# Kernel tuning notes

Measured on AMD Instinct MI355X. Metric: run time of the kernel, lower is better.

The kernel has to match this reference:

```python
import jax, jax.numpy as jnp
import numpy as np

D = 1024      # model_dim
H = 16        # n_heads
BLOCK = 256   # block_dim
B, S = 4, 4096


def setup_inputs() -> dict:
    key = jax.random.key(0)
    ks = jax.random.split(key, 6)
    x = jax.random.normal(ks[0], (B, S, D), dtype=jnp.float32)
    # random permutation per batch row (mirrors torch.argsort(torch.rand(...)))
    rand_perm = jnp.argsort(jax.random.uniform(ks[1], (B, S)), axis=-1).astype(jnp.int32)
    W_in = jax.random.normal(ks[2], (D, 3 * D), dtype=jnp.float32) / np.float32(np.sqrt(D))
    b_in = jax.random.normal(ks[3], (3 * D,), dtype=jnp.float32) * 0.02
    W_out = jax.random.normal(ks[4], (D, D), dtype=jnp.float32) / np.float32(np.sqrt(D))
    b_out = jax.random.normal(ks[5], (D,), dtype=jnp.float32) * 0.02
    return {"x": x, "rand_perm": rand_perm, "W_in": W_in, "b_in": b_in,
            "W_out": W_out, "b_out": b_out}


def reference(x, rand_perm, W_in, b_in, W_out, b_out):
    Bb, Ss, Dm = x.shape
    dh = Dm // H
    nb = Ss // BLOCK  # S divisible by BLOCK -> no padding needed
    # permute sequence: x_rand[..., i, :] = x[..., perm[i], :]
    x_r = jnp.take_along_axis(x, rand_perm[..., None], axis=-2)          # [B,S,D]
    xb = x_r.reshape(Bb, nb, BLOCK, Dm)                                   # block-diagonal chunks
    qkv = jnp.einsum('bntd,de->bnte', xb, W_in) + b_in                    # [B,nb,blk,3D]
    # torch layout: chunk by head first, then (q,k,v) within head
    qkv = qkv.reshape(Bb, nb, BLOCK, H, 3, dh)
    q = jnp.moveaxis(qkv[..., 0, :], 3, 2)                                # [B,nb,H,blk,dh]
    k = jnp.moveaxis(qkv[..., 1, :], 3, 2)
    v = jnp.moveaxis(qkv[..., 2, :], 3, 2)
    scores = jnp.einsum('bnhtd,bnhsd->bnhts', q, k) / np.float32(np.sqrt(dh))
    att = jax.nn.softmax(scores, axis=-1)
    o = jnp.einsum('bnhts,bnhsd->bnhtd', att, v)                          # [B,nb,H,blk,dh]

    def merge(t):  # [B,nb,H,blk,dh] -> [B,S,D] (heads concatenated on feature dim)
        return jnp.moveaxis(t, 2, 3).reshape(Bb, Ss, Dm)

    o = merge(o) @ W_out + b_out
    k_f = merge(k)
    v_f = merge(v)
    # scatter back: out[perm[i]] = src[i]  <=>  out[j] = src[inv_perm[j]]
    inv = jnp.argsort(rand_perm, axis=-1)
    unperm = lambda t: jnp.take_along_axis(t, inv[..., None], axis=-2)
    return unperm(o), unperm(k_f), unperm(v_f)
```

## Files before the change

kernel.cpp:

```cpp
#include <hip/hip_runtime.h>

#define D_   1024
#define H_   16
#define DHd  64
#define BLK  256
#define B_   4
#define S_   4096
#define NB_  16
#define M_   16384
#define N1_  3072
#define NT_  32

typedef __attribute__((ext_vector_type(8))) short short8;
typedef __attribute__((ext_vector_type(4))) float f32x4;
typedef unsigned short u16;
typedef __attribute__((ext_vector_type(4))) unsigned short u16x4;

__device__ inline u16 f2bf(float f) {
  unsigned int u = __float_as_uint(f);
  unsigned int r = (u + 0x7fffu + ((u >> 16) & 1u)) >> 16;
  return (u16)r;
}

__device__ inline void async_ld16(const void* g, void* l) {
  __builtin_amdgcn_global_load_lds(
      (const __attribute__((address_space(1))) unsigned int*)g,
      (__attribute__((address_space(3))) unsigned int*)l, 16, 0, 0);
}

__global__ __launch_bounds__(256)
void permute_cast_kernel(const float* __restrict__ x, const int* __restrict__ perm,
                         u16* __restrict__ xp) {
  int bid = blockIdx.x;
  int b = bid >> 12;
  int i = bid & 4095;
  int prow = perm[b * S_ + i];
  const float4* src = reinterpret_cast<const float4*>(x + (size_t)(b * S_ + prow) * D_);
  float4 v = src[threadIdx.x];
  u16x4 o;
  o.x = f2bf(v.x); o.y = f2bf(v.y); o.z = f2bf(v.z); o.w = f2bf(v.w);
  reinterpret_cast<u16x4*>(xp + (size_t)bid * D_)[threadIdx.x] = o;
}

__global__ __launch_bounds__(256)
void transpose_cast_kernel(const float* __restrict__ src, u16* __restrict__ dst,
                           int R, int C) {
  __shared__ float tile[32][33];
  int tx = threadIdx.x, ty = threadIdx.y;
  int c0 = blockIdx.x * 32, r0 = blockIdx.y * 32;
  #pragma unroll
  for (int i = ty; i < 32; i += 8)
    tile[i][tx] = src[(size_t)(r0 + i) * C + c0 + tx];
  __syncthreads();
  #pragma unroll
  for (int i = ty; i < 32; i += 8)
    dst[(size_t)(c0 + i) * R + r0 + tx] = f2bf(tile[tx][i]);
}

template<int MODE>
__global__ __launch_bounds__(512, 2)
void gemm_kernel(const u16* __restrict__ A, const u16* __restrict__ BT,
                 const float* __restrict__ bias, const int* __restrict__ perm,
                 u16* __restrict__ q_ws, u16* __restrict__ k_ws, u16* __restrict__ vT_ws,
                 float* __restrict__ out_k, float* __restrict__ out_v,
                 float* __restrict__ out_o) {
  constexpr int NCOL = (MODE == 0) ? N1_ : D_;
  constexpr int NWG  = (M_ / 256) * (NCOL / 256);
  constexpr int CPX  = NWG / 8;

  __shared__ u16 LDS[4 * 16384];
  __shared__ int perm_l[256];

  const int tid  = threadIdx.x;
  const int lane = tid & 63;
  const int w    = tid >> 6;
  const int wr   = w >> 2, wc = w & 3;
  const int l4   = lane >> 4, l15 = lane & 15;

  const int orig = blockIdx.x;
  const int lid  = (orig & 7) * CPX + (orig >> 3);
  const int i0   = (lid & 63) * 256;
  const int n0   = (lid >> 6) * 256;
  const int bidx = i0 >> 12;

  if (tid < 256) perm_l[tid] = perm[bidx * S_ + (i0 & 4095) + tid];

  const int srow = tid >> 2;
  const int sq   = (tid & 3) ^ ((tid >> 3) & 3);
  const u16* pA0 = A  + (size_t)(i0 + srow) * 1024 + sq * 8;
  const u16* pA1 = pA0 + (size_t)128 * 1024;
  const u16* pB0 = BT + (size_t)(n0 + srow) * 1024 + sq * 8;
  const u16* pB1 = pB0 + (size_t)128 * 1024;

  const int ps   = l4 ^ ((l15 >> 1) & 3);
  const int aoff = (wr * 128 + l15) * 64 + ps * 16;
  const int boff = 16384 + (wc * 64 + l15) * 64 + ps * 16;

  f32x4 acc[8][4] = {};

  #define STAGE(kt, b) do {                                    \
    const int ko_ = (kt) * 32;                                 \
    u16* base_ = &LDS[(b) * 16384 + w * 512];                  \
    async_ld16(pA0 + ko_, base_);                              \
    async_ld16(pA1 + ko_, base_ + 4096);                       \
    async_ld16(pB0 + ko_, base_ + 8192);                       \
    async_ld16(pB1 + ko_, base_ + 12288);                      \
  } while (0)

  #define COMPUTE(b) do {                                                         \
    const char* lb_ = (const char*)LDS + (b) * 32768;                             \
    short8 af_[8], bf_[4];                                                        \
    _Pragma("unroll")                                                             \
    for (int m = 0; m < 8; ++m)                                                   \
      af_[m] = *reinterpret_cast<const short8*>(lb_ + aoff + m * 1024);           \
    bf_[0] = *reinterpret_cast<const short8*>(lb_ + boff);                        \
    bf_[1] = *reinterpret_cast<const short8*>(lb_ + boff + 1024);                 \
    __builtin_amdgcn_s_setprio(1);                                                \
    _Pragma("unroll")                                                             \
    for (int m = 0; m < 8; ++m) {                                                 \
      acc[m][0] = __builtin_amdgcn_mfma_f32_16x16x32_bf16(af_[m], bf_[0], acc[m][0], 0, 0, 0); \
      acc[m][1] = __builtin_amdgcn_mfma_f32_16x16x32_bf16(af_[m], bf_[1], acc[m][1], 0, 0, 0); \
    }                                                                             \
    __builtin_amdgcn_s_setprio(0);                                                \
    bf_[2] = *reinterpret_cast<const short8*>(lb_ + boff + 2048);                 \
    bf_[3] = *reinterpret_cast<const short8*>(lb_ + boff + 3072);                 \
    __builtin_amdgcn_s_setprio(1);                                                \
    _Pragma("unroll")                                                             \
    for (int m = 0; m < 8; ++m) {                                                 \
      acc[m][2] = __builtin_amdgcn_mfma_f32_16x16x32_bf16(af_[m], bf_[2], acc[m][2], 0, 0, 0); \
      acc[m][3] = __builtin_amdgcn_mfma_f32_16x16x32_bf16(af_[m], bf_[3], acc[m][3], 0, 0, 0); \
    }                                                                             \
    __builtin_amdgcn_s_setprio(0);                                                \
  } while (0)

  STAGE(0, 0);
  STAGE(1, 1);
  #pragma unroll 1
  for (int kt = 0; kt < NT_ - 2; ++kt) {
    STAGE(kt + 2, (kt + 2) & 3);
    asm volatile("s_waitcnt vmcnt(8) lgkmcnt(0)" ::: "memory");
    __builtin_amdgcn_s_barrier();
    COMPUTE(kt & 3);
  }
  asm volatile("s_waitcnt vmcnt(4) lgkmcnt(0)" ::: "memory");
  __builtin_amdgcn_s_barrier();
  COMPUTE((NT_ - 2) & 3);
  asm volatile("s_waitcnt vmcnt(0) lgkmcnt(0)" ::: "memory");
  __builtin_amdgcn_s_barrier();
  COMPUTE((NT_ - 1) & 3);
  #undef STAGE
  #undef COMPUTE

  if (MODE == 0) {
    #pragma unroll
    for (int n = 0; n < 4; ++n) {
      int col = n0 + wc * 64 + n * 16 + l15;
      float bias_v = bias[col];
      int h  = col / 192;
      int rem = col - h * 192;
      int cc = rem >> 6;
      int dd = rem & 63;
      int qcol = (h << 6) + dd;
      #pragma unroll
      for (int m = 0; m < 8; ++m) {
        int rbase = i0 + wr * 128 + m * 16 + l4 * 4;
        if (cc == 0) {
          #pragma unroll
          for (int r = 0; r < 4; ++r) {
            float val = acc[m][n][r] + bias_v;
            q_ws[(size_t)(rbase + r) * D_ + qcol] = f2bf(val);
          }
        } else if (cc == 1) {
          #pragma unroll
          for (int r = 0; r < 4; ++r) {
            float val = acc[m][n][r] + bias_v;
            int rr = rbase + r;
            k_ws[(size_t)rr * D_ + qcol] = f2bf(val);
            int prow = perm_l[rr - i0];
            out_k[(size_t)(bidx * S_ + prow) * D_ + qcol] = val;
          }
        } else {
          u16x4 pk;
          #pragma unroll
          for (int r = 0; r < 4; ++r) {
            float val = acc[m][n][r] + bias_v;
            int rr = rbase + r;
            int prow = perm_l[rr - i0];
            out_v[(size_t)(bidx * S_ + prow) * D_ + qcol] = val;
            pk[r] = f2bf(val);
          }
          int i_loc = rbase & 4095;
          int nblk = i_loc >> 8;
          int t    = i_loc & 255;
          *reinterpret_cast<u16x4*>(
              &vT_ws[((((size_t)bidx * NB_ + nblk) * H_ + h) * DHd + dd) * BLK + t]) = pk;
        }
      }
    }
  } else {
    #pragma unroll
    for (int n = 0; n < 4; ++n) {
      int col = n0 + wc * 64 + n * 16 + l15;
      float bias_v = bias[col];
      #pragma unroll
      for (int m = 0; m < 8; ++m) {
        int rbase = i0 + wr * 128 + m * 16 + l4 * 4;
        #pragma unroll
        for (int r = 0; r < 4; ++r) {
          int rr = rbase + r;
          int prow = perm_l[rr - i0];
          out_o[(size_t)(bidx * S_ + prow) * D_ + col] = acc[m][n][r] + bias_v;
        }
      }
    }
  }
}

__global__ __launch_bounds__(256)
void attn_kernel(const u16* __restrict__ q_ws, const u16* __restrict__ k_ws,
                 const u16* __restrict__ vT_ws, u16* __restrict__ o_ws) {
  __shared__ u16 P_lds[4 * 64 * 64];

  int bid  = blockIdx.x;
  int h    = bid & 15;
  int nblk = (bid >> 4) & 15;
  int b    = bid >> 8;
  int row0 = b * S_ + nblk * BLK;
  int lane = threadIdx.x & 63;
  int w    = threadIdx.x >> 6;
  int l4 = lane >> 4, l15 = lane & 15;

  const u16* qb  = q_ws + (size_t)row0 * D_ + h * 64;
  const u16* kb  = k_ws + (size_t)row0 * D_ + h * 64;
  const u16* vTb = vT_ws + ((size_t)(b * NB_ + nblk) * H_ + h) * (size_t)(DHd * BLK);

  short8 qf[4][2];
  #pragma unroll
  for (int mt = 0; mt < 4; ++mt)
    #pragma unroll
    for (int kk = 0; kk < 2; ++kk)
      qf[mt][kk] = *reinterpret_cast<const short8*>(
          qb + (size_t)(w * 64 + mt * 16 + l15) * D_ + kk * 32 + l4 * 8);

  f32x4 Oacc[4][4] = {};
  float mS[4][4], lS[4][4];
  #pragma unroll
  for (int mt = 0; mt < 4; ++mt)
    #pragma unroll
    for (int r = 0; r < 4; ++r) { mS[mt][r] = -1e30f; lS[mt][r] = 0.f; }

  for (int ct = 0; ct < 4; ++ct) {
    f32x4 Sc[4][4] = {};
    #pragma unroll
    for (int kk = 0; kk < 2; ++kk) {
      #pragma unroll
      for (int nt = 0; nt < 4; ++nt) {
        short8 kf = *reinterpret_cast<const short8*>(
            kb + (size_t)(ct * 64 + nt * 16 + l15) * D_ + kk * 32 + l4 * 8);
        #pragma unroll
        for (int mt = 0; mt < 4; ++mt)
          Sc[mt][nt] = __builtin_amdgcn_mfma_f32_16x16x32_bf16(qf[mt][kk], kf, Sc[mt][nt], 0, 0, 0);
      }
    }
    #pragma unroll
    for (int mt = 0; mt < 4; ++mt) {
      #pragma unroll
      for (int r = 0; r < 4; ++r) {
        float v0 = fmaxf(fmaxf(Sc[mt][0][r], Sc[mt][1][r]), fmaxf(Sc[mt][2][r], Sc[mt][3][r]));
        v0 *= 0.125f;
        v0 = fmaxf(v0, __shfl_xor(v0, 1));
        v0 = fmaxf(v0, __shfl_xor(v0, 2));
        v0 = fmaxf(v0, __shfl_xor(v0, 4));
        v0 = fmaxf(v0, __shfl_xor(v0, 8));
        float mn = fmaxf(mS[mt][r], v0);
        float alpha = __expf(mS[mt][r] - mn);
        mS[mt][r] = mn;
        float rs = 0.f;
        #pragma unroll
        for (int nt = 0; nt < 4; ++nt) {
          float p = __expf(Sc[mt][nt][r] * 0.125f - mn);
          Sc[mt][nt][r] = p;
          rs += p;
        }
        rs += __shfl_xor(rs, 1);
        rs += __shfl_xor(rs, 2);
        rs += __shfl_xor(rs, 4);
        rs += __shfl_xor(rs, 8);
        lS[mt][r] = lS[mt][r] * alpha + rs;
        #pragma unroll
        for (int nt = 0; nt < 4; ++nt)
          Oacc[mt][nt][r] *= alpha;
      }
    }
    #pragma unroll
    for (int mt = 0; mt < 4; ++mt)
      #pragma unroll
      for (int nt = 0; nt < 4; ++nt)
        #pragma unroll
        for (int r = 0; r < 4; ++r)
          P_lds[w * 4096 + (mt * 16 + l4 * 4 + r) * 64 + nt * 16 + l15] = f2bf(Sc[mt][nt][r]);
    #pragma unroll
    for (int kk = 0; kk < 2; ++kk) {
      short8 pa[4];
      #pragma unroll
      for (int mt = 0; mt < 4; ++mt)
        pa[mt] = *reinterpret_cast<const short8*>(
            &P_lds[w * 4096 + (mt * 16 + l15) * 64 + kk * 32 + l4 * 8]);
      #pragma unroll
      for (int nt = 0; nt < 4; ++nt) {
        short8 vf = *reinterpret_cast<const short8*>(
            vTb + (size_t)(nt * 16 + l15) * BLK + ct * 64 + kk * 32 + l4 * 8);
        #pragma unroll
        for (int mt = 0; mt < 4; ++mt)
          Oacc[mt][nt] = __builtin_amdgcn_mfma_f32_16x16x32_bf16(pa[mt], vf, Oacc[mt][nt], 0, 0, 0);
      }
    }
  }
  u16* ob = o_ws + (size_t)row0 * D_ + h * 64;
  #pragma unroll
  for (int mt = 0; mt < 4; ++mt)
    #pragma unroll
    for (int r = 0; r < 4; ++r) {
      float inv = 1.f / lS[mt][r];
      int row = w * 64 + mt * 16 + l4 * 4 + r;
      #pragma unroll
      for (int nt = 0; nt < 4; ++nt)
        ob[(size_t)row * D_ + nt * 16 + l15] = f2bf(Oacc[mt][nt][r] * inv);
    }
}

extern "C" void kernel_launch(void* const* d_in, const int* in_sizes, int n_in,
                              void* d_out, int out_size, void* d_ws, size_t ws_size,
                              hipStream_t stream) {
  const float* x     = (const float*)d_in[0];
  const int*   perm  = (const int*)d_in[1];
  const float* W_in  = (const float*)d_in[2];
  const float* b_in  = (const float*)d_in[3];
  const float* W_out = (const float*)d_in[4];
  const float* b_out = (const float*)d_in[5];

  float* out_o = (float*)d_out;
  float* out_k = out_o + (size_t)M_ * D_;
  float* out_v = out_k + (size_t)M_ * D_;

  const size_t nE = (size_t)M_ * D_;
  u16 *xp, *q_ws, *k_ws, *vT, *o_ws, *WinT, *WoutT;
  size_t need_full = (5 * nE + (size_t)N1_ * D_ + (size_t)D_ * D_) * 2;
  if (ws_size >= need_full) {
    u16* w = (u16*)d_ws;
    xp = w; q_ws = xp + nE; k_ws = q_ws + nE; vT = k_ws + nE; o_ws = vT + nE;
    WinT = o_ws + nE; WoutT = WinT + (size_t)N1_ * D_;
  } else {
    xp = (u16*)d_out; q_ws = xp + nE;
    u16* w = (u16*)d_ws;
    k_ws = w; vT = k_ws + nE; o_ws = vT + nE;
    WinT = o_ws + nE; WoutT = WinT + (size_t)N1_ * D_;
  }

  permute_cast_kernel<<<M_, 256, 0, stream>>>(x, perm, xp);
  transpose_cast_kernel<<<dim3(N1_ / 32, D_ / 32), dim3(32, 8), 0, stream>>>(W_in, WinT, D_, N1_);
  transpose_cast_kernel<<<dim3(D_ / 32, D_ / 32), dim3(32, 8), 0, stream>>>(W_out, WoutT, D_, D_);
  gemm_kernel<0><<<(M_ / 256) * (N1_ / 256), 512, 0, stream>>>(
      xp, WinT, b_in, perm, q_ws, k_ws, vT, out_k, out_v, nullptr);
  attn_kernel<<<B_ * NB_ * H_, 256, 0, stream>>>(q_ws, k_ws, vT, o_ws);
  gemm_kernel<1><<<(M_ / 256) * (D_ / 256), 512, 0, stream>>>(
      o_ws, WoutT, b_out, perm, nullptr, nullptr, nullptr, nullptr, nullptr, out_o);
}
```

Before: 322.8 us.

## Restructure GEMM main loop into 8-wave ping-pong subtiles with deeper prefetch

Reworks the GEMM K-loop so each K-tile is processed in two half-M subtiles, with async global-to-LDS loads for A and B split and interleaved between the MFMA phases. Raw s_barrier instructions are placed between phases so the waves stay in lockstep, and the prefetch depth grows from two to three tiles ahead. The goal is to overlap memory traffic with MFMA work and keep fewer register fragments live. The trade-off is more barriers per tile and fragile hand-tuned vmcnt accounting.

```diff
diff --git a/kernel.cpp b/kernel.cpp
--- a/kernel.cpp
+++ b/kernel.cpp
@@ -98,58 +98,80 @@
 
   f32x4 acc[8][4] = {};
 
-  #define STAGE(kt, b) do {                                    \
-    const int ko_ = (kt) * 32;                                 \
-    u16* base_ = &LDS[(b) * 16384 + w * 512];                  \
-    async_ld16(pA0 + ko_, base_);                              \
-    async_ld16(pA1 + ko_, base_ + 4096);                       \
-    async_ld16(pB0 + ko_, base_ + 8192);                       \
-    async_ld16(pB1 + ko_, base_ + 12288);                      \
+  #define STAGE_A(kt, b) do {                                  \
+    u16* dA_ = &LDS[(b) * 16384 + w * 512];                    \
+    const int koA_ = (kt) * 32;                                \
+    async_ld16(pA0 + koA_, dA_);                               \
+    async_ld16(pA1 + koA_, dA_ + 4096);                        \
   } while (0)
-
-  #define COMPUTE(b) do {                                                         \
-    const char* lb_ = (const char*)LDS + (b) * 32768;                             \
-    short8 af_[8], bf_[4];                                                        \
-    _Pragma("unroll")                                                             \
-    for (int m = 0; m < 8; ++m)                                                   \
+  #define STAGE_B(kt, b) do {                                  \
+    u16* dB_ = &LDS[(b) * 16384 + 8192 + w * 512];             \
+    const int koB_ = (kt) * 32;                                \
+    async_ld16(pB0 + koB_, dB_);                               \
+    async_ld16(pB1 + koB_, dB_ + 4096);                        \
+  } while (0)
+  #define NOPST ((void)0)
+
+  #define SUBTILE(BUF, STGA, STGB, VMSTMT) do {                                   \
+    const char* lb_ = (const char*)LDS + (BUF) * 32768;                           \
+    short8 af_[4], bf_[4];                                                        \
+                                                        \
+    _Pragma("unroll")                                                             \
+    for (int m = 0; m < 4; ++m)                                                   \
       af_[m] = *reinterpret_cast<const short8*>(lb_ + aoff + m * 1024);           \
-    bf_[0] = *reinterpret_cast<const short8*>(lb_ + boff);                        \
-    bf_[1] = *reinterpret_cast<const short8*>(lb_ + boff + 1024);                 \
+    _Pragma("unroll")                                                             \
+    for (int n = 0; n < 4; ++n)                                                   \
+      bf_[n] = *reinterpret_cast<const short8*>(lb_ + boff + n * 1024);           \
+    STGA;                                                                         \
+    asm volatile("s_barrier" ::: "memory");                                       \
+    asm volatile("s_waitcnt lgkmcnt(0)" ::: "memory");                            \
     __builtin_amdgcn_s_setprio(1);                                                \
     _Pragma("unroll")                                                             \
-    for (int m = 0; m < 8; ++m) {                                                 \
-      acc[m][0] = __builtin_amdgcn_mfma_f32_16x16x32_bf16(af_[m], bf_[0], acc[m][0], 0, 0, 0); \
-      acc[m][1] = __builtin_amdgcn_mfma_f32_16x16x32_bf16(af_[m], bf_[1], acc[m][1], 0, 0, 0); \
-    }                                                                             \
+    for (int m = 0; m < 4; ++m)                                                   \
+      _Pragma("unroll")                                                           \
+      for (int n = 0; n < 4; ++n)                                                 \
+        acc[m][n] = __builtin_amdgcn_mfma_f32_16x16x32_bf16(af_[m], bf_[n], acc[m][n], 0, 0, 0); \
     __builtin_amdgcn_s_setprio(0);                                                \
-    bf_[2] = *reinterpret_cast<const short8*>(lb_ + boff + 2048);                 \
-    bf_[3] = *reinterpret_cast<const short8*>(lb_ + boff + 3072);                 \
+    asm volatile("s_barrier" ::: "memory");                                       \
+                                                        \
+    _Pragma("unroll")                                                             \
+    for (int m = 0; m < 4; ++m)                                                   \
+      af_[m] = *reinterpret_cast<const short8*>(lb_ + aoff + (m + 4) * 1024);     \
+    STGB;                                                                         \
+    asm volatile("s_barrier" ::: "memory");                                       \
+    asm volatile("s_waitcnt lgkmcnt(0)" ::: "memory");                            \
     __builtin_amdgcn_s_setprio(1);                                                \
     _Pragma("unroll")                                                             \
-    for (int m = 0; m < 8; ++m) {                                                 \
-      acc[m][2] = __builtin_amdgcn_mfma_f32_16x16x32_bf16(af_[m], bf_[2], acc[m][2], 0, 0, 0); \
-      acc[m][3] = __builtin_amdgcn_mfma_f32_16x16x32_bf16(af_[m], bf_[3], acc[m][3], 0, 0, 0); \
-    }                                                                             \
+    for (int m = 0; m < 4; ++m)                                                   \
+      _Pragma("unroll")                                                           \
+      for (int n = 0; n < 4; ++n)                                                 \
+        acc[m + 4][n] = __builtin_amdgcn_mfma_f32_16x16x32_bf16(af_[m], bf_[n], acc[m + 4][n], 0, 0, 0); \
     __builtin_amdgcn_s_setprio(0);                                                \
+    VMSTMT;                                                                       \
+    asm volatile("s_barrier" ::: "memory");                                       \
   } while (0)
 
-  STAGE(0, 0);
-  STAGE(1, 1);
-  #pragma unroll 1
-  for (int kt = 0; kt < NT_ - 2; ++kt) {
-    STAGE(kt + 2, (kt + 2) & 3);
-    asm volatile("s_waitcnt vmcnt(8) lgkmcnt(0)" ::: "memory");
-    __builtin_amdgcn_s_barrier();
-    COMPUTE(kt & 3);
+  STAGE_A(0, 0); STAGE_B(0, 0);
+  STAGE_A(1, 1); STAGE_B(1, 1);
+  STAGE_A(2, 2); STAGE_B(2, 2);
+  asm volatile("s_waitcnt vmcnt(8)" ::: "memory");
+  asm volatile("s_barrier" ::: "memory");
+
+  #pragma unroll 4
+  for (int t = 0; t < NT_ - 4; ++t) {
+    SUBTILE((t & 3), STAGE_A(t + 3, (t + 3) & 3), STAGE_B(t + 3, (t + 3) & 3),
+            asm volatile("s_waitcnt vmcnt(8)" ::: "memory"));
   }
-  asm volatile("s_waitcnt vmcnt(4) lgkmcnt(0)" ::: "memory");
-  __builtin_amdgcn_s_barrier();
-  COMPUTE((NT_ - 2) & 3);
-  asm volatile("s_waitcnt vmcnt(0) lgkmcnt(0)" ::: "memory");
-  __builtin_amdgcn_s_barrier();
-  COMPUTE((NT_ - 1) & 3);
-  #undef STAGE
-  #undef COMPUTE
+  SUBTILE(0, STAGE_A(31, 3), STAGE_B(31, 3),
+          asm volatile("s_waitcnt vmcnt(8)" ::: "memory"));
+  SUBTILE(1, NOPST, NOPST, asm volatile("s_waitcnt vmcnt(4)" ::: "memory"));
+  SUBTILE(2, NOPST, NOPST, asm volatile("s_waitcnt vmcnt(0)" ::: "memory"));
+  SUBTILE(3, NOPST, NOPST, NOPST);
+
+  #undef SUBTILE
+  #undef STAGE_A
+  #undef STAGE_B
+  #undef NOPST
 
   if (MODE == 0) {
     #pragma unroll
```

Result: slower. 339.2 us (+5.1%).

## Move K/V fp32 scatter out of QKV GEMM epilogue into attention kernel

Applied to the files above, without the earlier changes.

The QKV GEMM epilogue no longer writes scattered fp32 K (and V when workspace allows) rows. It writes bf16 copies instead, and the attention kernel afterwards reads those copies and emits the unpermuted fp32 outputs as vectorised float4 rows. The GEMM tile mapping also changes from column-major to row-major panel order. The aim is to take strided 4-byte scatter stores off the GEMM's critical epilogue. The cost is extra bf16 reads and writes, and the fp32 K/V outputs are now rounded through bf16, which loses precision.

```diff
diff --git a/kernel.cpp b/kernel.cpp
--- a/kernel.cpp
+++ b/kernel.cpp
@@ -21,6 +21,7 @@
   unsigned int r = (u + 0x7fffu + ((u >> 16) & 1u)) >> 16;
   return (u16)r;
 }
+__device__ inline float bf2f(u16 v) { return __uint_as_float(((unsigned)v) << 16); }
 
 __device__ inline void async_ld16(const void* g, void* l) {
   __builtin_amdgcn_global_load_lds(
@@ -57,15 +58,16 @@
     dst[(size_t)(c0 + i) * R + r0 + tx] = f2bf(tile[tx][i]);
 }
 
-template<int MODE>
+template<int MODE, bool VDIRECT>
 __global__ __launch_bounds__(512, 2)
 void gemm_kernel(const u16* __restrict__ A, const u16* __restrict__ BT,
                  const float* __restrict__ bias, const int* __restrict__ perm,
-                 u16* __restrict__ q_ws, u16* __restrict__ k_ws, u16* __restrict__ vT_ws,
-                 float* __restrict__ out_k, float* __restrict__ out_v,
+                 u16* __restrict__ q_ws, u16* __restrict__ k_ws, u16* __restrict__ v_ws,
+                 u16* __restrict__ vT_ws, float* __restrict__ out_v,
                  float* __restrict__ out_o) {
   constexpr int NCOL = (MODE == 0) ? N1_ : D_;
-  constexpr int NWG  = (M_ / 256) * (NCOL / 256);
+  constexpr int NPAN = NCOL / 256;
+  constexpr int NWG  = (M_ / 256) * NPAN;
   constexpr int CPX  = NWG / 8;
 
   __shared__ u16 LDS[4 * 16384];
@@ -79,11 +81,13 @@
 
   const int orig = blockIdx.x;
   const int lid  = (orig & 7) * CPX + (orig >> 3);
-  const int i0   = (lid & 63) * 256;
-  const int n0   = (lid >> 6) * 256;
+  const int i0   = (lid / NPAN) * 256;
+  const int n0   = (lid % NPAN) * 256;
   const int bidx = i0 >> 12;
 
-  if (tid < 256) perm_l[tid] = perm[bidx * S_ + (i0 & 4095) + tid];
+  if (MODE == 1 || VDIRECT) {
+    if (tid < 256) perm_l[tid] = perm[bidx * S_ + (i0 & 4095) + tid];
+  }
 
   const int srow = tid >> 2;
   const int sq   = (tid & 3) ^ ((tid >> 3) & 3);
@@ -166,28 +170,24 @@
         int rbase = i0 + wr * 128 + m * 16 + l4 * 4;
         if (cc == 0) {
           #pragma unroll
-          for (int r = 0; r < 4; ++r) {
-            float val = acc[m][n][r] + bias_v;
-            q_ws[(size_t)(rbase + r) * D_ + qcol] = f2bf(val);
-          }
+          for (int r = 0; r < 4; ++r)
+            q_ws[(size_t)(rbase + r) * D_ + qcol] = f2bf(acc[m][n][r] + bias_v);
         } else if (cc == 1) {
           #pragma unroll
-          for (int r = 0; r < 4; ++r) {
-            float val = acc[m][n][r] + bias_v;
-            int rr = rbase + r;
-            k_ws[(size_t)rr * D_ + qcol] = f2bf(val);
-            int prow = perm_l[rr - i0];
-            out_k[(size_t)(bidx * S_ + prow) * D_ + qcol] = val;
-          }
+          for (int r = 0; r < 4; ++r)
+            k_ws[(size_t)(rbase + r) * D_ + qcol] = f2bf(acc[m][n][r] + bias_v);
         } else {
           u16x4 pk;
           #pragma unroll
           for (int r = 0; r < 4; ++r) {
             float val = acc[m][n][r] + bias_v;
-            int rr = rbase + r;
-            int prow = perm_l[rr - i0];
-            out_v[(size_t)(bidx * S_ + prow) * D_ + qcol] = val;
             pk[r] = f2bf(val);
+            if (VDIRECT) {
+              int prow = perm_l[rbase + r - i0];
+              out_v[(size_t)(bidx * S_ + prow) * D_ + qcol] = val;
+            } else {
+              v_ws[(size_t)(rbase + r) * D_ + qcol] = pk[r];
+            }
           }
           int i_loc = rbase & 4095;
           int nblk = i_loc >> 8;
@@ -216,9 +216,12 @@
   }
 }
 
+template<bool COPYV>
 __global__ __launch_bounds__(256)
 void attn_kernel(const u16* __restrict__ q_ws, const u16* __restrict__ k_ws,
-                 const u16* __restrict__ vT_ws, u16* __restrict__ o_ws) {
+                 const u16* __restrict__ v_ws, const u16* __restrict__ vT_ws,
+                 u16* __restrict__ o_ws, const int* __restrict__ perm,
+                 float* __restrict__ out_k, float* __restrict__ out_v) {
   __shared__ u16 P_lds[4 * 64 * 64];
 
   int bid  = blockIdx.x;
@@ -327,6 +330,34 @@
       for (int nt = 0; nt < 4; ++nt)
         ob[(size_t)row * D_ + nt * 16 + l15] = f2bf(Oacc[mt][nt][r] * inv);
     }
+
+  const int rowg = threadIdx.x >> 2;
+  const int cseg = (threadIdx.x & 3) << 4;
+  #pragma unroll
+  for (int it = 0; it < 4; ++it) {
+    int rr = rowg + it * 64;
+    int prow = perm[b * S_ + nblk * BLK + rr];
+    size_t soff = (size_t)(row0 + rr) * D_ + h * 64 + cseg;
+    size_t doff = (size_t)(b * S_ + prow) * D_ + h * 64 + cseg;
+    {
+      short8 a = *reinterpret_cast<const short8*>(k_ws + soff);
+      short8 c = *reinterpret_cast<const short8*>(k_ws + soff + 8);
+      float4* dst = reinterpret_cast<float4*>(out_k + doff);
+      dst[0] = make_float4(bf2f((u16)a[0]), bf2f((u16)a[1]), bf2f((u16)a[2]), bf2f((u16)a[3]));
+      dst[1] = make_float4(bf2f((u16)a[4]), bf2f((u16)a[5]), bf2f((u16)a[6]), bf2f((u16)a[7]));
+      dst[2] = make_float4(bf2f((u16)c[0]), bf2f((u16)c[1]), bf2f((u16)c[2]), bf2f((u16)c[3]));
+      dst[3] = make_float4(bf2f((u16)c[4]), bf2f((u16)c[5]), bf2f((u16)c[6]), bf2f((u16)c[7]));
+    }
+    if (COPYV) {
+      short8 a = *reinterpret_cast<const short8*>(v_ws + soff);
+      short8 c = *reinterpret_cast<const short8*>(v_ws + soff + 8);
+      float4* dst = reinterpret_cast<float4*>(out_v + doff);
+      dst[0] = make_float4(bf2f((u16)a[0]), bf2f((u16)a[1]), bf2f((u16)a[2]), bf2f((u16)a[3]));
+      dst[1] = make_float4(bf2f((u16)a[4]), bf2f((u16)a[5]), bf2f((u16)a[6]), bf2f((u16)a[7]));
+      dst[2] = make_float4(bf2f((u16)c[0]), bf2f((u16)c[1]), bf2f((u16)c[2]), bf2f((u16)c[3]));
+      dst[3] = make_float4(bf2f((u16)c[4]), bf2f((u16)c[5]), bf2f((u16)c[6]), bf2f((u16)c[7]));
+    }
+  }
 }
 
 extern "C" void kernel_launch(void* const* d_in, const int* in_sizes, int n_in,
@@ -343,26 +374,43 @@
   float* out_k = out_o + (size_t)M_ * D_;
   float* out_v = out_k + (size_t)M_ * D_;
 
-  const size_t nE = (size_t)M_ * D_;
-  u16 *xp, *q_ws, *k_ws, *vT, *o_ws, *WinT, *WoutT;
-  size_t need_full = (5 * nE + (size_t)N1_ * D_ + (size_t)D_ * D_) * 2;
-  if (ws_size >= need_full) {
-    u16* w = (u16*)d_ws;
-    xp = w; q_ws = xp + nE; k_ws = q_ws + nE; vT = k_ws + nE; o_ws = vT + nE;
+  const size_t nE  = (size_t)M_ * D_;
+  const size_t MiB = (size_t)1 << 20;
+  u16 *xp, *q_ws, *k_ws, *v_ws, *vT, *o_ws, *WinT, *WoutT;
+  bool vws;
+  u16* w = (u16*)d_ws;
+  u16* park = (u16*)d_out;
+
+  if (ws_size >= 202 * MiB) {
+    vws = true;
+    xp = w; q_ws = xp + nE; k_ws = q_ws + nE; v_ws = k_ws + nE; vT = v_ws + nE;
+    o_ws = vT + nE; WinT = o_ws + nE; WoutT = WinT + (size_t)N1_ * D_;
+  } else if (ws_size >= 138 * MiB) {
+    vws = true;
+    xp = park; q_ws = park + nE;
+    k_ws = w; v_ws = k_ws + nE; vT = v_ws + nE; o_ws = vT + nE;
     WinT = o_ws + nE; WoutT = WinT + (size_t)N1_ * D_;
   } else {
-    xp = (u16*)d_out; q_ws = xp + nE;
-    u16* w = (u16*)d_ws;
-    k_ws = w; vT = k_ws + nE; o_ws = vT + nE;
+    vws = false;
+    xp = park; q_ws = park + nE;
+    k_ws = w; v_ws = nullptr; vT = k_ws + nE; o_ws = vT + nE;
     WinT = o_ws + nE; WoutT = WinT + (size_t)N1_ * D_;
   }
 
   permute_cast_kernel<<<M_, 256, 0, stream>>>(x, perm, xp);
   transpose_cast_kernel<<<dim3(N1_ / 32, D_ / 32), dim3(32, 8), 0, stream>>>(W_in, WinT, D_, N1_);
   transpose_cast_kernel<<<dim3(D_ / 32, D_ / 32), dim3(32, 8), 0, stream>>>(W_out, WoutT, D_, D_);
-  gemm_kernel<0><<<(M_ / 256) * (N1_ / 256), 512, 0, stream>>>(
-      xp, WinT, b_in, perm, q_ws, k_ws, vT, out_k, out_v, nullptr);
-  attn_kernel<<<B_ * NB_ * H_, 256, 0, stream>>>(q_ws, k_ws, vT, o_ws);
-  gemm_kernel<1><<<(M_ / 256) * (D_ / 256), 512, 0, stream>>>(
+  if (vws) {
+    gemm_kernel<0, false><<<(M_ / 256) * (N1_ / 256), 512, 0, stream>>>(
+        xp, WinT, b_in, perm, q_ws, k_ws, v_ws, vT, nullptr, nullptr);
+    attn_kernel<true><<<B_ * NB_ * H_, 256, 0, stream>>>(
+        q_ws, k_ws, v_ws, vT, o_ws, perm, out_k, out_v);
+  } else {
+    gemm_kernel<0, true><<<(M_ / 256) * (N1_ / 256), 512, 0, stream>>>(
+        xp, WinT, b_in, perm, q_ws, k_ws, nullptr, vT, out_v, nullptr);
+    attn_kernel<false><<<B_ * NB_ * H_, 256, 0, stream>>>(
+        q_ws, k_ws, nullptr, vT, o_ws, perm, out_k, nullptr);
+  }
+  gemm_kernel<1, false><<<(M_ / 256) * (D_ / 256), 512, 0, stream>>>(
       o_ws, WoutT, b_out, perm, nullptr, nullptr, nullptr, nullptr, nullptr, out_o);
 }
```

New measurement: 360.1 us. 11.6% more time.

## Restructure GEMM mainloop to BK=64 double-buffered pipeline with XOR swizzle

Applied to the files above, without the earlier changes.

Changes the GEMM K-tile from 32 to 64, going from a 4-stage ring with 2-deep prefetch to a 2-stage double buffer that issues the next tile's load before computing the current one. It uses a new 8-way XOR LDS swizzle, reorders tile indexing so consecutive workgroups walk N-panels first, and loads all A and B fragments before 32 back-to-back MFMAs per k-substep. It drops the occupancy hint of 2 blocks per CU, which allows more registers per thread but means only one block fits per CU given the 128KB of LDS.

```diff
diff --git a/kernel.cpp b/kernel.cpp
--- a/kernel.cpp
+++ b/kernel.cpp
@@ -9,7 +9,7 @@
 #define NB_  16
 #define M_   16384
 #define N1_  3072
-#define NT_  32
+#define KT_  16
 
 typedef __attribute__((ext_vector_type(8))) short short8;
 typedef __attribute__((ext_vector_type(4))) float f32x4;
@@ -58,17 +58,18 @@
 }
 
 template<int MODE>
-__global__ __launch_bounds__(512, 2)
+__global__ __launch_bounds__(512)
 void gemm_kernel(const u16* __restrict__ A, const u16* __restrict__ BT,
                  const float* __restrict__ bias, const int* __restrict__ perm,
                  u16* __restrict__ q_ws, u16* __restrict__ k_ws, u16* __restrict__ vT_ws,
                  float* __restrict__ out_k, float* __restrict__ out_v,
                  float* __restrict__ out_o) {
   constexpr int NCOL = (MODE == 0) ? N1_ : D_;
-  constexpr int NWG  = (M_ / 256) * (NCOL / 256);
+  constexpr int NPAN = NCOL / 256;
+  constexpr int NWG  = (M_ / 256) * NPAN;
   constexpr int CPX  = NWG / 8;
 
-  __shared__ u16 LDS[4 * 16384];
+  __shared__ u16 LDS[2 * 32768];
   __shared__ int perm_l[256];
 
   const int tid  = threadIdx.x;
@@ -79,75 +80,71 @@
 
   const int orig = blockIdx.x;
   const int lid  = (orig & 7) * CPX + (orig >> 3);
-  const int i0   = (lid & 63) * 256;
-  const int n0   = (lid >> 6) * 256;
+  const int i0   = (lid / NPAN) * 256;
+  const int n0   = (lid % NPAN) * 256;
   const int bidx = i0 >> 12;
 
   if (tid < 256) perm_l[tid] = perm[bidx * S_ + (i0 & 4095) + tid];
 
-  const int srow = tid >> 2;
-  const int sq   = (tid & 3) ^ ((tid >> 3) & 3);
-  const u16* pA0 = A  + (size_t)(i0 + srow) * 1024 + sq * 8;
-  const u16* pA1 = pA0 + (size_t)128 * 1024;
-  const u16* pB0 = BT + (size_t)(n0 + srow) * 1024 + sq * 8;
-  const u16* pB1 = pB0 + (size_t)128 * 1024;
-
-  const int ps   = l4 ^ ((l15 >> 1) & 3);
-  const int aoff = (wr * 128 + l15) * 64 + ps * 16;
-  const int boff = 16384 + (wc * 64 + l15) * 64 + ps * 16;
+  const int sl8 = (((lane & 7) ^ (lane >> 3)) << 3);
+  const u16* pA = A  + (size_t)(i0 + w * 8 + (lane >> 3)) * 1024 + sl8;
+  const u16* pB = BT + (size_t)(n0 + w * 8 + (lane >> 3)) * 1024 + sl8;
+
+  const int pk0 = ((l4)     ^ (l15 & 7)) * 16;
+  const int pk1 = ((4 + l4) ^ (l15 & 7)) * 16;
+  const int abase = (wr * 128 + l15) * 128;
+  const int bbase = 32768 + (wc * 64 + l15) * 128;
 
   f32x4 acc[8][4] = {};
 
   #define STAGE(kt, b) do {                                    \
-    const int ko_ = (kt) * 32;                                 \
-    u16* base_ = &LDS[(b) * 16384 + w * 512];                  \
-    async_ld16(pA0 + ko_, base_);                              \
-    async_ld16(pA1 + ko_, base_ + 4096);                       \
-    async_ld16(pB0 + ko_, base_ + 8192);                       \
-    async_ld16(pB1 + ko_, base_ + 12288);                      \
+    const size_t ko_ = (size_t)(kt) * 64;                      \
+    u16* d_ = &LDS[(b) * 32768 + w * 512];                     \
+    async_ld16(pA + ko_,              d_);                     \
+    async_ld16(pA + ko_ +  64 * 1024, d_ + 4096);              \
+    async_ld16(pA + ko_ + 128 * 1024, d_ + 8192);              \
+    async_ld16(pA + ko_ + 192 * 1024, d_ + 12288);             \
+    async_ld16(pB + ko_,              d_ + 16384);             \
+    async_ld16(pB + ko_ +  64 * 1024, d_ + 20480);             \
+    async_ld16(pB + ko_ + 128 * 1024, d_ + 24576);             \
+    async_ld16(pB + ko_ + 192 * 1024, d_ + 28672);             \
   } while (0)
 
   #define COMPUTE(b) do {                                                         \
-    const char* lb_ = (const char*)LDS + (b) * 32768;                             \
-    short8 af_[8], bf_[4];                                                        \
+    const char* lb_ = (const char*)LDS + (b) * 65536;                             \
     _Pragma("unroll")                                                             \
-    for (int m = 0; m < 8; ++m)                                                   \
-      af_[m] = *reinterpret_cast<const short8*>(lb_ + aoff + m * 1024);           \
-    bf_[0] = *reinterpret_cast<const short8*>(lb_ + boff);                        \
-    bf_[1] = *reinterpret_cast<const short8*>(lb_ + boff + 1024);                 \
-    __builtin_amdgcn_s_setprio(1);                                                \
-    _Pragma("unroll")                                                             \
-    for (int m = 0; m < 8; ++m) {                                                 \
-      acc[m][0] = __builtin_amdgcn_mfma_f32_16x16x32_bf16(af_[m], bf_[0], acc[m][0], 0, 0, 0); \
-      acc[m][1] = __builtin_amdgcn_mfma_f32_16x16x32_bf16(af_[m], bf_[1], acc[m][1], 0, 0, 0); \
+    for (int kk = 0; kk < 2; ++kk) {                                              \
+      const int pk_ = kk ? pk1 : pk0;                                             \
+      short8 af_[8], bf_[4];                                                      \
+      _Pragma("unroll")                                                           \
+      for (int m = 0; m < 8; ++m)                                                 \
+        af_[m] = *reinterpret_cast<const short8*>(lb_ + abase + m * 2048 + pk_);  \
+      _Pragma("unroll")                                                           \
+      for (int n = 0; n < 4; ++n)                                                 \
+        bf_[n] = *reinterpret_cast<const short8*>(lb_ + bbase + n * 2048 + pk_);  \
+      asm volatile("s_waitcnt lgkmcnt(0)" ::: "memory");                          \
+      __builtin_amdgcn_sched_barrier(0);                                          \
+      __builtin_amdgcn_s_setprio(1);                                              \
+      _Pragma("unroll")                                                           \
+      for (int m = 0; m < 8; ++m)                                                 \
+        _Pragma("unroll")                                                         \
+        for (int n = 0; n < 4; ++n)                                               \
+          acc[m][n] = __builtin_amdgcn_mfma_f32_16x16x32_bf16(af_[m], bf_[n], acc[m][n], 0, 0, 0); \
+      __builtin_amdgcn_s_setprio(0);                                              \
     }                                                                             \
-    __builtin_amdgcn_s_setprio(0);                                                \
-    bf_[2] = *reinterpret_cast<const short8*>(lb_ + boff + 2048);                 \
-    bf_[3] = *reinterpret_cast<const short8*>(lb_ + boff + 3072);                 \
-    __builtin_amdgcn_s_setprio(1);                                                \
-    _Pragma("unroll")                                                             \
-    for (int m = 0; m < 8; ++m) {                                                 \
-      acc[m][2] = __builtin_amdgcn_mfma_f32_16x16x32_bf16(af_[m], bf_[2], acc[m][2], 0, 0, 0); \
-      acc[m][3] = __builtin_amdgcn_mfma_f32_16x16x32_bf16(af_[m], bf_[3], acc[m][3], 0, 0, 0); \
-    }                                                                             \
-    __builtin_amdgcn_s_setprio(0);                                                \
   } while (0)
 
   STAGE(0, 0);
-  STAGE(1, 1);
-  #pragma unroll 1
-  for (int kt = 0; kt < NT_ - 2; ++kt) {
-    STAGE(kt + 2, (kt + 2) & 3);
-    asm volatile("s_waitcnt vmcnt(8) lgkmcnt(0)" ::: "memory");
+  asm volatile("s_waitcnt vmcnt(0)" ::: "memory");
+  __builtin_amdgcn_s_barrier();
+  #pragma unroll 2
+  for (int kt = 0; kt < KT_ - 1; ++kt) {
+    STAGE(kt + 1, (kt + 1) & 1);
+    COMPUTE(kt & 1);
+    asm volatile("s_waitcnt vmcnt(0)" ::: "memory");
     __builtin_amdgcn_s_barrier();
-    COMPUTE(kt & 3);
   }
-  asm volatile("s_waitcnt vmcnt(4) lgkmcnt(0)" ::: "memory");
-  __builtin_amdgcn_s_barrier();
-  COMPUTE((NT_ - 2) & 3);
-  asm volatile("s_waitcnt vmcnt(0) lgkmcnt(0)" ::: "memory");
-  __builtin_amdgcn_s_barrier();
-  COMPUTE((NT_ - 1) & 3);
+  COMPUTE((KT_ - 1) & 1);
   #undef STAGE
   #undef COMPUTE
 
@@ -166,10 +163,8 @@
         int rbase = i0 + wr * 128 + m * 16 + l4 * 4;
         if (cc == 0) {
           #pragma unroll
-          for (int r = 0; r < 4; ++r) {
-            float val = acc[m][n][r] + bias_v;
-            q_ws[(size_t)(rbase + r) * D_ + qcol] = f2bf(val);
-          }
+          for (int r = 0; r < 4; ++r)
+            q_ws[(size_t)(rbase + r) * D_ + qcol] = f2bf(acc[m][n][r] + bias_v);
         } else if (cc == 1) {
           #pragma unroll
           for (int r = 0; r < 4; ++r) {
```

After: 398.5 us. 23.4% more time.
